# Optimization experiments

Hardware: AMD Instinct MI355X
Metric: run time of the kernel (lower is better)

The kernel has to match this reference:

```python
import jax, jax.numpy as jnp
import numpy as np


def setup_inputs() -> dict:
    key = jax.random.key(0)
    ks = jax.random.split(key, 8)
    B, T, U = 4, 400, 80
    De, Dd, V = 512, 512, 1024
    F = De + Dd  # in_features = 1024
    s = lambda k, shape: jax.random.normal(k, shape, dtype=jnp.float32) * 0.05
    return {
        "encoder_output": jax.random.normal(ks[0], (B, T, De), dtype=jnp.float32),
        "decoder_output": jax.random.normal(ks[1], (B, U, Dd), dtype=jnp.float32),
        "W_enc": s(ks[2], (F, De)),
        "b_enc": s(ks[3], (F,)),
        "W_dec": s(ks[4], (F, Dd)),
        "b_dec": s(ks[5], (F,)),
        "W_fc": s(ks[6], (V, F)),
        "b_fc": s(ks[7], (V,)),
    }


def reference(encoder_output, decoder_output, W_enc, b_enc, W_dec, b_dec, W_fc, b_fc):
    # fc_enc / fc_dec projections: (B,T,F) and (B,U,F)
    enc = jnp.einsum("btd,fd->btf", encoder_output, W_enc) + b_enc
    dec = jnp.einsum("bud,fd->buf", decoder_output, W_dec) + b_dec
    # broadcast-add -> (B,T,U,F)
    combined = enc[:, :, None, :] + dec[:, None, :, :]
    # fc: tanh then linear -> (B,T,U,V)
    vocab_logits = jnp.einsum("btuf,vf->btuv", jnp.tanh(combined), W_fc) + b_fc
    # HAT branch: blank prob via sigmoid of logit 0
    blk_logit = vocab_logits[..., :1]
    log_blk = jax.nn.log_sigmoid(blk_logit)          # log(sigmoid)
    log_not_blk = jax.nn.log_sigmoid(-blk_logit)     # log(1 - sigmoid)
    vocab_log_probs = log_not_blk + jax.nn.log_softmax(vocab_logits[..., 1:], axis=-1)
    return jnp.concatenate([log_blk, vocab_log_probs], axis=-1)
```

## Files before the change

kernel.cpp:

```cpp
#include <hip/hip_runtime.h>
#include <hip/hip_bf16.h>
#include <cstdint>
#include <cstddef>

typedef short bf16x8 __attribute__((ext_vector_type(8)));
typedef float f32x4 __attribute__((ext_vector_type(4)));

static __device__ __forceinline__ unsigned short f2bf(float f) {
    union { float f; uint32_t u; } c; c.f = f;
    uint32_t r = c.u + 0x7FFFu + ((c.u >> 16) & 1u);
    return (unsigned short)(r >> 16);
}
static __device__ __forceinline__ float bf2f_lo(uint32_t w) {
    union { uint32_t u; float f; } c; c.u = w << 16; return c.f;
}
static __device__ __forceinline__ float bf2f_hi(uint32_t w) {
    union { uint32_t u; float f; } c; c.u = w & 0xffff0000u; return c.f;
}
static __device__ __forceinline__ float fast_tanh(float x) {
    float e = __expf(2.0f * x);
    return 1.0f - 2.0f / (e + 1.0f);
}
static __device__ __forceinline__ float softplus_f(float x) {
    return fmaxf(x, 0.0f) + log1pf(__expf(-fabsf(x)));
}

#define GLOAD_LDS16(g, l) \
    __builtin_amdgcn_global_load_lds((const __attribute__((address_space(1))) void*)(g), \
                                     (__attribute__((address_space(3))) void*)(l), 16, 0, 0)

__global__ __launch_bounds__(256) void k_convert(
    const float* __restrict__ s0, const float* __restrict__ s1,
    const float* __restrict__ s2, const float* __restrict__ s3,
    const float* __restrict__ s4,
    unsigned short* __restrict__ d0, unsigned short* __restrict__ d1,
    unsigned short* __restrict__ d2, unsigned short* __restrict__ d3,
    unsigned short* __restrict__ d4,
    int n0, int n1, int n2, int n3, int n4)
{
    int i = blockIdx.x * 256 + threadIdx.x;
    int c0 = n0 >> 2, c1 = c0 + (n1 >> 2), c2 = c1 + (n2 >> 2),
        c3 = c2 + (n3 >> 2), c4 = c3 + (n4 >> 2);
    if (i >= c4) return;
    const float* s; unsigned short* d; int j;
    if (i < c0)      { s = s0; d = d0; j = i; }
    else if (i < c1) { s = s1; d = d1; j = i - c0; }
    else if (i < c2) { s = s2; d = d2; j = i - c1; }
    else if (i < c3) { s = s3; d = d3; j = i - c2; }
    else             { s = s4; d = d4; j = i - c3; }
    float4 v = reinterpret_cast<const float4*>(s)[j];
    ushort4 o;
    o.x = f2bf(v.x); o.y = f2bf(v.y); o.z = f2bf(v.z); o.w = f2bf(v.w);
    reinterpret_cast<ushort4*>(d)[j] = o;
}

__global__ __launch_bounds__(256) void k_proj(
    const unsigned short* __restrict__ A,
    const unsigned short* __restrict__ W,
    const float* __restrict__ bias,
    float* __restrict__ out)
{
    __shared__ unsigned short As[32 * 512];
    const int tid = threadIdx.x;
    const int m0 = blockIdx.x * 32;
    const int c0 = blockIdx.y * 128;
    {
        int row = tid >> 3;
        const unsigned short* src = A + (size_t)(m0 + row) * 512;
        unsigned int base = row * 1024;
        unsigned int sw = (row & 7) << 4;
        #pragma unroll
        for (int c = 0; c < 8; ++c) {
            int col = (tid & 7) * 8 + c * 64;
            bf16x8 v = *reinterpret_cast<const bf16x8*>(src + col);
            *reinterpret_cast<bf16x8*>(
                reinterpret_cast<char*>(As) + ((base + col * 2) ^ sw)) = v;
        }
    }
    __syncthreads();
    const int w = tid >> 6, l = tid & 63;
    const int lr = l & 15, lkb = (l >> 4) * 8;
    f32x4 acc[2][2] = {};
    const int colbase = c0 + w * 32;
    const unsigned short* Wb = W + (size_t)(colbase + lr) * 512 + lkb;
    const unsigned int sw = (lr & 7) << 4;
    for (int ks = 0; ks < 16; ++ks) {
        unsigned int kb = (ks * 32 + lkb) * 2;
        bf16x8 a0 = *reinterpret_cast<const bf16x8*>(
            reinterpret_cast<const char*>(As) + ((lr * 1024 + kb) ^ sw));
        bf16x8 a1 = *reinterpret_cast<const bf16x8*>(
            reinterpret_cast<const char*>(As) + (((16 + lr) * 1024 + kb) ^ sw));
        #pragma unroll
        for (int nf = 0; nf < 2; ++nf) {
            bf16x8 b = *reinterpret_cast<const bf16x8*>(Wb + nf * 16 * 512 + ks * 32);
            acc[0][nf] = __builtin_amdgcn_mfma_f32_16x16x32_bf16(a0, b, acc[0][nf], 0, 0, 0);
            acc[1][nf] = __builtin_amdgcn_mfma_f32_16x16x32_bf16(a1, b, acc[1][nf], 0, 0, 0);
        }
    }
    const int qr = (l >> 4) * 4;
    #pragma unroll
    for (int nf = 0; nf < 2; ++nf) {
        int col = colbase + nf * 16 + lr;
        float bv = bias[col];
        #pragma unroll
        for (int mf = 0; mf < 2; ++mf)
            #pragma unroll
            for (int r = 0; r < 4; ++r)
                out[(size_t)(m0 + mf * 16 + qr + r) * 1024 + col] = acc[mf][nf][r] + bv;
    }
}

__global__ __launch_bounds__(256) void k_tanhA(
    const float* __restrict__ enc_f,
    const float* __restrict__ dec_f,
    char* __restrict__ outb)
{
    const int NG = 128000 * 128;
    for (int g = blockIdx.x * 256 + threadIdx.x; g < NG; g += gridDim.x * 256) {
        int row = g >> 7, c8 = g & 127;
        int bt = row / 80;
        int u = row - bt * 80;
        int b = bt / 400;
        const float* ep = enc_f + (size_t)bt * 1024 + c8 * 8;
        const float* dp = dec_f + (size_t)(b * 80 + u) * 1024 + c8 * 8;
        float4 e0 = *(const float4*)ep, e1 = *(const float4*)(ep + 4);
        float4 f0 = *(const float4*)dp, f1 = *(const float4*)(dp + 4);
        uint4 pk;
        pk.x = (uint32_t)f2bf(fast_tanh(e0.x + f0.x)) | ((uint32_t)f2bf(fast_tanh(e0.y + f0.y)) << 16);
        pk.y = (uint32_t)f2bf(fast_tanh(e0.z + f0.z)) | ((uint32_t)f2bf(fast_tanh(e0.w + f0.w)) << 16);
        pk.z = (uint32_t)f2bf(fast_tanh(e1.x + f1.x)) | ((uint32_t)f2bf(fast_tanh(e1.y + f1.y)) << 16);
        pk.w = (uint32_t)f2bf(fast_tanh(e1.z + f1.z)) | ((uint32_t)f2bf(fast_tanh(e1.w + f1.w)) << 16);
        *(uint4*)(outb + (size_t)row * 4096 + c8 * 16) = pk;
    }
}

__global__ __launch_bounds__(512, 1) void k_gemm(
    const unsigned short* __restrict__ Wfc,
    const float* __restrict__ bfc,
    char* __restrict__ outb)
{
    extern __shared__ char smem[];
    const int tid = threadIdx.x;
    const int w = tid >> 6, l = tid & 63;
    const int lr = l & 15, q = l >> 4;
    const int wm = w >> 2, wn = w & 3;

    const int bid = (int)blockIdx.x;
    const int g = (bid & 7) * 250 + (bid >> 3);
    const size_t R0 = (size_t)(g >> 2) * 256;
    const int n0 = (g & 3) * 256;

    const unsigned kb0 = (unsigned)(((tid & 7) * 16) ^ (((tid >> 3) & 7) << 4));
    const int row0 = tid >> 3;
    const char* sA = outb + (R0 + row0) * 4096 + kb0;
    const char* sB = (const char*)Wfc + (size_t)(n0 + row0) * 2048 + kb0;
    char* const dbase = smem + tid * 16;

#define STG_A(buf, T) do { \
    const char* _a = sA + (T) * 128; char* _d = dbase + (buf); \
    GLOAD_LDS16(_a,          _d);          \
    GLOAD_LDS16(_a + 262144, _d + 8192);   \
    GLOAD_LDS16(_a + 524288, _d + 16384);  \
    GLOAD_LDS16(_a + 786432, _d + 24576);  \
} while (0)
#define STG_B01(buf, T) do { const char* _b = sB + (T) * 128; char* _d = dbase + (buf); \
    GLOAD_LDS16(_b,          _d + 32768); GLOAD_LDS16(_b + 131072, _d + 40960); } while (0)
#define STG_B23(buf, T) do { const char* _b = sB + (T) * 128; char* _d = dbase + (buf); \
    GLOAD_LDS16(_b + 262144, _d + 49152); GLOAD_LDS16(_b + 393216, _d + 57344); } while (0)

    const unsigned key = (unsigned)((lr & 7) << 4);
    const unsigned kx0 = (unsigned)(q * 16) ^ key;
    const unsigned kx1 = (unsigned)(q * 16 + 64) ^ key;
    const unsigned abase = (unsigned)((wm * 128 + lr) * 128);
    const unsigned bbase = (unsigned)(32768 + (wn * 64 + lr) * 128);

    f32x4 acc[8][4] = {};
    bf16x8 af[4][2], bf[4][2];

#define LDA(h) do { \
    _Pragma("unroll") \
    for (int mf = 0; mf < 4; ++mf) { \
        const char* _p = smem + cb + abase + (h) * 8192 + mf * 2048; \
        af[mf][0] = *(const bf16x8*)(_p + kx0); \
        af[mf][1] = *(const bf16x8*)(_p + kx1); \
    } } while (0)
#define LDB(gg) do { \
    _Pragma("unroll") \
    for (int j = 0; j < 2; ++j) { \
        const char* _p = smem + cb + bbase + ((gg) * 2 + j) * 2048; \
        bf[(gg) * 2 + j][0] = *(const bf16x8*)(_p + kx0); \
        bf[(gg) * 2 + j][1] = *(const bf16x8*)(_p + kx1); \
    } } while (0)
#define MFQ(h, gg) do { \
    __builtin_amdgcn_s_setprio(1); \
    _Pragma("unroll") \
    for (int j = 0; j < 2; ++j) \
        _Pragma("unroll") \
        for (int ks = 0; ks < 2; ++ks) \
            _Pragma("unroll") \
            for (int mf = 0; mf < 4; ++mf) \
                acc[(h) * 4 + mf][(gg) * 2 + j] = __builtin_amdgcn_mfma_f32_16x16x32_bf16( \
                    bf[(gg) * 2 + j][ks], af[mf][ks], acc[(h) * 4 + mf][(gg) * 2 + j], 0, 0, 0); \
    __builtin_amdgcn_s_setprio(0); \
} while (0)
#define BAR __builtin_amdgcn_s_barrier()

    STG_A(0u, 0);
    STG_B01(0u, 0);
    STG_B23(0u, 0);
    STG_A(65536u, 1);
    asm volatile("s_waitcnt vmcnt(4)" ::: "memory");
    BAR;
    __builtin_amdgcn_sched_barrier(0);

    #pragma unroll 2
    for (int t = 0; t < 16; ++t) {
        const unsigned cb = (unsigned)(t & 1) * 65536u;
        const unsigned nb = cb ^ 65536u;
        const bool s1 = (t + 1 < 16), s2 = (t + 2 < 16);
        LDA(0); LDB(0);
        BAR;
        MFQ(0, 0);
        LDB(1);
        if (s1) STG_B01(nb, t + 1);
        BAR;
        MFQ(0, 1);
        LDA(1);
        if (s1) STG_B23(nb, t + 1);
        BAR;
        MFQ(1, 1);
        BAR;
        if (s2) STG_A(cb, t + 2);
        MFQ(1, 0);
        if (t < 14) {
            asm volatile("s_waitcnt vmcnt(4)" ::: "memory");
            BAR;
            __builtin_amdgcn_sched_barrier(0);
        } else if (t == 14) {
            asm volatile("s_waitcnt vmcnt(0)" ::: "memory");
            BAR;
            __builtin_amdgcn_sched_barrier(0);
        }
    }
#undef LDA
#undef LDB
#undef MFQ
#undef BAR
#undef STG_A
#undef STG_B01
#undef STG_B23

    #pragma unroll
    for (int nf = 0; nf < 4; ++nf) {
        const int v = n0 + wn * 64 + nf * 16 + q * 4;
        float4 bv = *(const float4*)(bfc + v);
        #pragma unroll
        for (int mf8 = 0; mf8 < 8; ++mf8) {
            f32x4 a = acc[mf8][nf];
            uint2 pk;
            pk.x = (uint32_t)f2bf(a[0] + bv.x) | ((uint32_t)f2bf(a[1] + bv.y) << 16);
            pk.y = (uint32_t)f2bf(a[2] + bv.z) | ((uint32_t)f2bf(a[3] + bv.w) << 16);
            size_t m = R0 + (size_t)(wm * 128 + mf8 * 16 + lr);
            *(uint2*)(outb + m * 4096 + 2048 + (size_t)v * 2) = pk;
        }
    }
}

__global__ __launch_bounds__(256) void k_softmax(char* __restrict__ outb)
{
    const int row = blockIdx.x * 4 + (threadIdx.x >> 6);
    const int l = threadIdx.x & 63;
    const char* lp = outb + (size_t)row * 4096 + 2048 + l * 32;
    uint4 wa = *(const uint4*)lp;
    uint4 wb = *(const uint4*)(lp + 16);
    float v[16];
    uint32_t wd[8] = { wa.x, wa.y, wa.z, wa.w, wb.x, wb.y, wb.z, wb.w };
    #pragma unroll
    for (int i = 0; i < 8; ++i) { v[2*i] = bf2f_lo(wd[i]); v[2*i+1] = bf2f_hi(wd[i]); }

    float l0 = __shfl(v[0], 0);
    float m = (l == 0) ? -3.0e38f : v[0];
    #pragma unroll
    for (int i = 1; i < 16; ++i) m = fmaxf(m, v[i]);
    #pragma unroll
    for (int s = 1; s < 64; s <<= 1) m = fmaxf(m, __shfl_xor(m, s));
    float s = (l == 0) ? 0.0f : __expf(v[0] - m);
    #pragma unroll
    for (int i = 1; i < 16; ++i) s += __expf(v[i] - m);
    #pragma unroll
    for (int sh = 1; sh < 64; sh <<= 1) s += __shfl_xor(s, sh);

    float lse = m + __logf(s);
    float fin = -lse - softplus_f(l0);
    float f0v = -softplus_f(-l0);

    float* op = (float*)(outb + (size_t)row * 4096) + l * 16;
    #pragma unroll
    for (int c = 0; c < 4; ++c) {
        float4 o;
        o.x = v[4*c+0] + fin; o.y = v[4*c+1] + fin;
        o.z = v[4*c+2] + fin; o.w = v[4*c+3] + fin;
        if (l == 0 && c == 0) o.x = f0v;
        *(float4*)(op + 4*c) = o;
    }
}

extern "C" void kernel_launch(void* const* d_in, const int* in_sizes, int n_in,
                              void* d_out, int out_size, void* d_ws, size_t ws_size,
                              hipStream_t stream)
{
    const float* encoder = (const float*)d_in[0];
    const float* decoder = (const float*)d_in[1];
    const float* W_enc   = (const float*)d_in[2];
    const float* b_enc   = (const float*)d_in[3];
    const float* W_dec   = (const float*)d_in[4];
    const float* b_dec   = (const float*)d_in[5];
    const float* W_fc    = (const float*)d_in[6];
    const float* b_fc    = (const float*)d_in[7];
    char* outb = (char*)d_out;

    char* ws = (char*)d_ws;
    float*          enc_f  = (float*)(ws);
    float*          dec_f  = (float*)(ws + 6553600);
    unsigned short* Wfc_h  = (unsigned short*)(ws + 7864320);
    unsigned short* Wenc_h = (unsigned short*)(ws + 9961472);
    unsigned short* Wdec_h = (unsigned short*)(ws + 11010048);
    unsigned short* encI_h = (unsigned short*)(ws + 12058624);
    unsigned short* decI_h = (unsigned short*)(ws + 13697024);

    const int nEnc = 4 * 400 * 512, nDec = 4 * 80 * 512;
    const int nWe = 1024 * 512, nWd = 1024 * 512, nWf = 1024 * 1024;
    const int totalF4 = (nEnc + nDec + nWe + nWd + nWf) >> 2;
    k_convert<<<(totalF4 + 255) / 256, 256, 0, stream>>>(
        encoder, decoder, W_enc, W_dec, W_fc,
        encI_h, decI_h, Wenc_h, Wdec_h, Wfc_h,
        nEnc, nDec, nWe, nWd, nWf);

    k_proj<<<dim3(1600 / 32, 8), 256, 0, stream>>>(encI_h, Wenc_h, b_enc, enc_f);
    k_proj<<<dim3(320 / 32, 8), 256, 0, stream>>>(decI_h, Wdec_h, b_dec, dec_f);

    k_tanhA<<<4096, 256, 0, stream>>>(enc_f, dec_f, outb);

    const int GEMM_SMEM = 131072;
    hipFuncSetAttribute(reinterpret_cast<const void*>(k_gemm),
                        hipFuncAttributeMaxDynamicSharedMemorySize, GEMM_SMEM);
    k_gemm<<<2000, 512, GEMM_SMEM, stream>>>(Wfc_h, b_fc, outb);

    k_softmax<<<32000, 256, 0, stream>>>(outb);
}
```

Baseline: 660.3 us.

## Double GEMM waves per block with smaller per-wave tiles; nontemporal softmax stores

Raises the GEMM block from 512 to 1024 threads. Each of the 16 waves now computes a 64x64 sub-tile of the 256x256 block tile instead of 128x64, and global-to-LDS staging and fragment loads are redistributed to match. The aim is more waves per CU to hide LDS and MFMA latency, at the cost of more barrier participants and a tighter per-thread register budget from the launch bound, which could cause spills. The softmax output write also switches to nontemporal stores to reduce cache pollution.

Measured after the change: 887.8 us. 34.5% more time.

```diff
diff --git a/kernel.cpp b/kernel.cpp
--- a/kernel.cpp
+++ b/kernel.cpp
@@ -134,7 +134,7 @@
     }
 }
 
-__global__ __launch_bounds__(512, 1) void k_gemm(
+__global__ __launch_bounds__(1024, 2) void k_gemm(
     const unsigned short* __restrict__ Wfc,
     const float* __restrict__ bfc,
     char* __restrict__ outb)
@@ -150,66 +150,63 @@
     const size_t R0 = (size_t)(g >> 2) * 256;
     const int n0 = (g & 3) * 256;
 
-    const unsigned kb0 = (unsigned)(((tid & 7) * 16) ^ (((tid >> 3) & 7) << 4));
-    const int row0 = tid >> 3;
-    const char* sA = outb + (R0 + row0) * 4096 + kb0;
-    const char* sB = (const char*)Wfc + (size_t)(n0 + row0) * 2048 + kb0;
+    const char* sA[2]; const char* sB[2];
+    #pragma unroll
+    for (int i = 0; i < 2; ++i) {
+        unsigned d = (unsigned)tid * 16 + i * 16384;
+        unsigned L = d ^ (((d >> 7) & 7u) << 4);
+        unsigned row = L >> 7, kb = L & 127u;
+        sA[i] = outb + (R0 + row) * 4096 + kb;
+        sB[i] = (const char*)Wfc + (size_t)(n0 + row) * 2048 + kb;
+    }
     char* const dbase = smem + tid * 16;
 
 #define STG_A(buf, T) do { \
-    const char* _a = sA + (T) * 128; char* _d = dbase + (buf); \
-    GLOAD_LDS16(_a,          _d);          \
-    GLOAD_LDS16(_a + 262144, _d + 8192);   \
-    GLOAD_LDS16(_a + 524288, _d + 16384);  \
-    GLOAD_LDS16(_a + 786432, _d + 24576);  \
+    GLOAD_LDS16(sA[0] + (T) * 128, dbase + (buf)); \
+    GLOAD_LDS16(sA[1] + (T) * 128, dbase + (buf) + 16384); \
 } while (0)
-#define STG_B01(buf, T) do { const char* _b = sB + (T) * 128; char* _d = dbase + (buf); \
-    GLOAD_LDS16(_b,          _d + 32768); GLOAD_LDS16(_b + 131072, _d + 40960); } while (0)
-#define STG_B23(buf, T) do { const char* _b = sB + (T) * 128; char* _d = dbase + (buf); \
-    GLOAD_LDS16(_b + 262144, _d + 49152); GLOAD_LDS16(_b + 393216, _d + 57344); } while (0)
+#define STG_B0(buf, T) do { \
+    GLOAD_LDS16(sB[0] + (T) * 128, dbase + (buf) + 32768); } while (0)
+#define STG_B1(buf, T) do { \
+    GLOAD_LDS16(sB[1] + (T) * 128, dbase + (buf) + 49152); } while (0)
 
     const unsigned key = (unsigned)((lr & 7) << 4);
     const unsigned kx0 = (unsigned)(q * 16) ^ key;
     const unsigned kx1 = (unsigned)(q * 16 + 64) ^ key;
-    const unsigned abase = (unsigned)((wm * 128 + lr) * 128);
+    const unsigned abase = (unsigned)((wm * 64 + lr) * 128);
     const unsigned bbase = (unsigned)(32768 + (wn * 64 + lr) * 128);
 
-    f32x4 acc[8][4] = {};
-    bf16x8 af[4][2], bf[4][2];
+    f32x4 acc[4][4] = {};
+    bf16x8 af[4], bfr[2];
 
 #define LDA(h) do { \
+    const unsigned _kx = (h) ? kx1 : kx0; \
     _Pragma("unroll") \
-    for (int mf = 0; mf < 4; ++mf) { \
-        const char* _p = smem + cb + abase + (h) * 8192 + mf * 2048; \
-        af[mf][0] = *(const bf16x8*)(_p + kx0); \
-        af[mf][1] = *(const bf16x8*)(_p + kx1); \
-    } } while (0)
-#define LDB(gg) do { \
-    _Pragma("unroll") \
-    for (int j = 0; j < 2; ++j) { \
-        const char* _p = smem + cb + bbase + ((gg) * 2 + j) * 2048; \
-        bf[(gg) * 2 + j][0] = *(const bf16x8*)(_p + kx0); \
-        bf[(gg) * 2 + j][1] = *(const bf16x8*)(_p + kx1); \
-    } } while (0)
-#define MFQ(h, gg) do { \
+    for (int mf = 0; mf < 4; ++mf) \
+        af[mf] = *(const bf16x8*)(smem + cb + abase + mf * 2048 + _kx); \
+} while (0)
+#define LDB2(h, gg) do { \
+    const unsigned _kx = (h) ? kx1 : kx0; \
+    bfr[0] = *(const bf16x8*)(smem + cb + bbase + ((gg) * 2 + 0) * 2048 + _kx); \
+    bfr[1] = *(const bf16x8*)(smem + cb + bbase + ((gg) * 2 + 1) * 2048 + _kx); \
+} while (0)
+#define MFQ(gg) do { \
     __builtin_amdgcn_s_setprio(1); \
     _Pragma("unroll") \
     for (int j = 0; j < 2; ++j) \
         _Pragma("unroll") \
-        for (int ks = 0; ks < 2; ++ks) \
-            _Pragma("unroll") \
-            for (int mf = 0; mf < 4; ++mf) \
-                acc[(h) * 4 + mf][(gg) * 2 + j] = __builtin_amdgcn_mfma_f32_16x16x32_bf16( \
-                    bf[(gg) * 2 + j][ks], af[mf][ks], acc[(h) * 4 + mf][(gg) * 2 + j], 0, 0, 0); \
+        for (int mf = 0; mf < 4; ++mf) \
+            acc[mf][(gg) * 2 + j] = __builtin_amdgcn_mfma_f32_16x16x32_bf16( \
+                bfr[j], af[mf], acc[mf][(gg) * 2 + j], 0, 0, 0); \
     __builtin_amdgcn_s_setprio(0); \
 } while (0)
 #define BAR __builtin_amdgcn_s_barrier()
 
     STG_A(0u, 0);
-    STG_B01(0u, 0);
-    STG_B23(0u, 0);
+    STG_B0(0u, 0);
+    STG_B1(0u, 0);
     STG_A(65536u, 1);
-    asm volatile("s_waitcnt vmcnt(4)" ::: "memory");
+    asm volatile("s_waitcnt vmcnt(2)" ::: "memory");
     BAR;
     __builtin_amdgcn_sched_barrier(0);
 
@@ -218,22 +215,23 @@
         const unsigned cb = (unsigned)(t & 1) * 65536u;
         const unsigned nb = cb ^ 65536u;
         const bool s1 = (t + 1 < 16), s2 = (t + 2 < 16);
-        LDA(0); LDB(0);
+        LDA(0); LDB2(0, 0);
         BAR;
-        MFQ(0, 0);
-        LDB(1);
-        if (s1) STG_B01(nb, t + 1);
+        MFQ(0);
+        LDB2(0, 1);
+        if (s1) STG_B0(nb, t + 1);
         BAR;
-        MFQ(0, 1);
-        LDA(1);
-        if (s1) STG_B23(nb, t + 1);
+        MFQ(1);
+        LDA(1); LDB2(1, 1);
+        if (s1) STG_B1(nb, t + 1);
         BAR;
-        MFQ(1, 1);
+        MFQ(1);
+        LDB2(1, 0);
         BAR;
         if (s2) STG_A(cb, t + 2);
-        MFQ(1, 0);
+        MFQ(0);
         if (t < 14) {
-            asm volatile("s_waitcnt vmcnt(4)" ::: "memory");
+            asm volatile("s_waitcnt vmcnt(2)" ::: "memory");
             BAR;
             __builtin_amdgcn_sched_barrier(0);
         } else if (t == 14) {
@@ -243,24 +241,24 @@
         }
     }
 #undef LDA
-#undef LDB
+#undef LDB2
 #undef MFQ
 #undef BAR
 #undef STG_A
-#undef STG_B01
-#undef STG_B23
+#undef STG_B0
+#undef STG_B1
 
     #pragma unroll
     for (int nf = 0; nf < 4; ++nf) {
         const int v = n0 + wn * 64 + nf * 16 + q * 4;
         float4 bv = *(const float4*)(bfc + v);
         #pragma unroll
-        for (int mf8 = 0; mf8 < 8; ++mf8) {
-            f32x4 a = acc[mf8][nf];
+        for (int mf = 0; mf < 4; ++mf) {
+            f32x4 a = acc[mf][nf];
             uint2 pk;
             pk.x = (uint32_t)f2bf(a[0] + bv.x) | ((uint32_t)f2bf(a[1] + bv.y) << 16);
             pk.y = (uint32_t)f2bf(a[2] + bv.z) | ((uint32_t)f2bf(a[3] + bv.w) << 16);
-            size_t m = R0 + (size_t)(wm * 128 + mf8 * 16 + lr);
+            size_t m = R0 + (size_t)(wm * 64 + mf * 16 + lr);
             *(uint2*)(outb + m * 4096 + 2048 + (size_t)v * 2) = pk;
         }
     }
@@ -297,11 +295,11 @@
     float* op = (float*)(outb + (size_t)row * 4096) + l * 16;
     #pragma unroll
     for (int c = 0; c < 4; ++c) {
-        float4 o;
-        o.x = v[4*c+0] + fin; o.y = v[4*c+1] + fin;
-        o.z = v[4*c+2] + fin; o.w = v[4*c+3] + fin;
-        if (l == 0 && c == 0) o.x = f0v;
-        *(float4*)(op + 4*c) = o;
+        f32x4 o;
+        o[0] = v[4*c+0] + fin; o[1] = v[4*c+1] + fin;
+        o[2] = v[4*c+2] + fin; o[3] = v[4*c+3] + fin;
+        if (l == 0 && c == 0) o[0] = f0v;
+        __builtin_nontemporal_store(o, (f32x4*)(op + 4*c));
     }
 }
 
@@ -344,7 +342,7 @@
     const int GEMM_SMEM = 131072;
     hipFuncSetAttribute(reinterpret_cast<const void*>(k_gemm),
                         hipFuncAttributeMaxDynamicSharedMemorySize, GEMM_SMEM);
-    k_gemm<<<2000, 512, GEMM_SMEM, stream>>>(Wfc_h, b_fc, outb);
+    k_gemm<<<2000, 1024, GEMM_SMEM, stream>>>(Wfc_h, b_fc, outb);
 
     k_softmax<<<32000, 256, 0, stream>>>(outb);
 }
```

## Restructure GEMM main loop with register double-buffered fragments and two waves per SIMD

Applied to the files above, without the earlier changes.

Rewrites the k_gemm pipeline so that A/B fragments for the next K-step are read from LDS during the current step, using separate register sets and a ping-pong B buffer. Global-to-LDS staging is regrouped into split A halves and a full B load, issued two tiles ahead, with adjusted vmcnt waits. Launch bounds change from 1 to 2 blocks per CU to allow more occupancy. The risks are higher register pressure under the tighter bound, which could cause spills given the 128 fp32 accumulators plus fragments, and more barriers per iteration. Two blocks at 128KB LDS each may also not fit on a CU, which would make the occupancy hint moot.

Measured after the change: 1.104 ms. 1.67x slower.

```diff
diff --git a/kernel.cpp b/kernel.cpp
--- a/kernel.cpp
+++ b/kernel.cpp
@@ -134,7 +134,7 @@
     }
 }
 
-__global__ __launch_bounds__(512, 1) void k_gemm(
+__global__ __launch_bounds__(512, 2) void k_gemm(
     const unsigned short* __restrict__ Wfc,
     const float* __restrict__ bfc,
     char* __restrict__ outb)
@@ -152,21 +152,27 @@
 
     const unsigned kb0 = (unsigned)(((tid & 7) * 16) ^ (((tid >> 3) & 7) << 4));
     const int row0 = tid >> 3;
-    const char* sA = outb + (R0 + row0) * 4096 + kb0;
-    const char* sB = (const char*)Wfc + (size_t)(n0 + row0) * 2048 + kb0;
+    const char* sA0 = outb + (R0 + row0) * 4096 + kb0;
+    const char* sB0 = (const char*)Wfc + (size_t)(n0 + row0) * 2048 + kb0;
     char* const dbase = smem + tid * 16;
 
-#define STG_A(buf, T) do { \
-    const char* _a = sA + (T) * 128; char* _d = dbase + (buf); \
-    GLOAD_LDS16(_a,          _d);          \
-    GLOAD_LDS16(_a + 262144, _d + 8192);   \
-    GLOAD_LDS16(_a + 524288, _d + 16384);  \
-    GLOAD_LDS16(_a + 786432, _d + 24576);  \
+#define STG_AF(buf, T) do { \
+    const char* _g = sA0 + (size_t)(T) * 128; \
+    GLOAD_LDS16(_g,          dbase + (buf)); \
+    GLOAD_LDS16(_g + 524288, dbase + (buf) + 16384); \
 } while (0)
-#define STG_B01(buf, T) do { const char* _b = sB + (T) * 128; char* _d = dbase + (buf); \
-    GLOAD_LDS16(_b,          _d + 32768); GLOAD_LDS16(_b + 131072, _d + 40960); } while (0)
-#define STG_B23(buf, T) do { const char* _b = sB + (T) * 128; char* _d = dbase + (buf); \
-    GLOAD_LDS16(_b + 262144, _d + 49152); GLOAD_LDS16(_b + 393216, _d + 57344); } while (0)
+#define STG_AS(buf, T) do { \
+    const char* _g = sA0 + (size_t)(T) * 128; \
+    GLOAD_LDS16(_g + 262144, dbase + (buf) + 8192); \
+    GLOAD_LDS16(_g + 786432, dbase + (buf) + 24576); \
+} while (0)
+#define STG_BALL(buf, T) do { \
+    const char* _g = sB0 + (size_t)(T) * 128; \
+    GLOAD_LDS16(_g,          dbase + (buf) + 32768); \
+    GLOAD_LDS16(_g + 131072, dbase + (buf) + 40960); \
+    GLOAD_LDS16(_g + 262144, dbase + (buf) + 49152); \
+    GLOAD_LDS16(_g + 393216, dbase + (buf) + 57344); \
+} while (0)
 
     const unsigned key = (unsigned)((lr & 7) << 4);
     const unsigned kx0 = (unsigned)(q * 16) ^ key;
@@ -174,93 +180,99 @@
     const unsigned abase = (unsigned)((wm * 128 + lr) * 128);
     const unsigned bbase = (unsigned)(32768 + (wn * 64 + lr) * 128);
 
+    bf16x8 a0f[8], a1f[8];
+    bf16x8 bp0[2][4], bp1[4];
     f32x4 acc[8][4] = {};
-    bf16x8 af[4][2], bf[4][2];
-
-#define LDA(h) do { \
+
+#define RD_A(dst, h, bufb) do { \
     _Pragma("unroll") \
-    for (int mf = 0; mf < 4; ++mf) { \
-        const char* _p = smem + cb + abase + (h) * 8192 + mf * 2048; \
-        af[mf][0] = *(const bf16x8*)(_p + kx0); \
-        af[mf][1] = *(const bf16x8*)(_p + kx1); \
+    for (int mf2 = 0; mf2 < 4; ++mf2) { \
+        const char* _p = smem + (bufb) + abase + (h) * 8192 + mf2 * 2048; \
+        dst[mf2 * 2 + 0] = *(const bf16x8*)(_p + kx0); \
+        dst[mf2 * 2 + 1] = *(const bf16x8*)(_p + kx1); \
     } } while (0)
-#define LDB(gg) do { \
+#define RD_B(dst, p, bufb) do { \
     _Pragma("unroll") \
     for (int j = 0; j < 2; ++j) { \
-        const char* _p = smem + cb + bbase + ((gg) * 2 + j) * 2048; \
-        bf[(gg) * 2 + j][0] = *(const bf16x8*)(_p + kx0); \
-        bf[(gg) * 2 + j][1] = *(const bf16x8*)(_p + kx1); \
+        const char* _p = smem + (bufb) + bbase + ((p) * 2 + j) * 2048; \
+        dst[j * 2 + 0] = *(const bf16x8*)(_p + kx0); \
+        dst[j * 2 + 1] = *(const bf16x8*)(_p + kx1); \
     } } while (0)
-#define MFQ(h, gg) do { \
+#define MFQ(h, p, aset, bset) do { \
     __builtin_amdgcn_s_setprio(1); \
     _Pragma("unroll") \
     for (int j = 0; j < 2; ++j) \
         _Pragma("unroll") \
         for (int ks = 0; ks < 2; ++ks) \
             _Pragma("unroll") \
-            for (int mf = 0; mf < 4; ++mf) \
-                acc[(h) * 4 + mf][(gg) * 2 + j] = __builtin_amdgcn_mfma_f32_16x16x32_bf16( \
-                    bf[(gg) * 2 + j][ks], af[mf][ks], acc[(h) * 4 + mf][(gg) * 2 + j], 0, 0, 0); \
+            for (int mf2 = 0; mf2 < 4; ++mf2) \
+                acc[(h) * 4 + mf2][(p) * 2 + j] = __builtin_amdgcn_mfma_f32_16x16x32_bf16( \
+                    bset[j * 2 + ks], aset[mf2 * 2 + ks], acc[(h) * 4 + mf2][(p) * 2 + j], 0, 0, 0); \
     __builtin_amdgcn_s_setprio(0); \
 } while (0)
 #define BAR __builtin_amdgcn_s_barrier()
 
-    STG_A(0u, 0);
-    STG_B01(0u, 0);
-    STG_B23(0u, 0);
-    STG_A(65536u, 1);
-    asm volatile("s_waitcnt vmcnt(4)" ::: "memory");
+    STG_AF(0u, 0); STG_BALL(0u, 0); STG_AS(0u, 0);
+    STG_AF(65536u, 1); STG_BALL(65536u, 1); STG_AS(65536u, 1);
+    asm volatile("s_waitcnt vmcnt(8)" ::: "memory");
     BAR;
     __builtin_amdgcn_sched_barrier(0);
+    RD_A(a0f, 0, 0u);
+    RD_B(bp0[0], 0, 0u);
 
     #pragma unroll 2
     for (int t = 0; t < 16; ++t) {
         const unsigned cb = (unsigned)(t & 1) * 65536u;
-        const unsigned nb = cb ^ 65536u;
-        const bool s1 = (t + 1 < 16), s2 = (t + 2 < 16);
-        LDA(0); LDB(0);
-        BAR;
-        MFQ(0, 0);
-        LDB(1);
-        if (s1) STG_B01(nb, t + 1);
-        BAR;
-        MFQ(0, 1);
-        LDA(1);
-        if (s1) STG_B23(nb, t + 1);
-        BAR;
-        MFQ(1, 1);
-        BAR;
-        if (s2) STG_A(cb, t + 2);
-        MFQ(1, 0);
+        const unsigned ob = cb ^ 65536u;
+        const bool s2 = (t + 2 < 16);
+        RD_B(bp1, 1, cb);
+        BAR;
+        MFQ(0, 0, a0f, bp0[t & 1]);
+        BAR;
+        RD_A(a1f, 1, cb);
+        if (s2) STG_AF(cb, t + 2);
+        BAR;
+        MFQ(0, 1, a0f, bp1);
+        BAR;
+        if (s2) STG_BALL(cb, t + 2);
+        BAR;
+        MFQ(1, 1, a1f, bp1);
+        BAR;
         if (t < 14) {
-            asm volatile("s_waitcnt vmcnt(4)" ::: "memory");
-            BAR;
-            __builtin_amdgcn_sched_barrier(0);
-        } else if (t == 14) {
+            asm volatile("s_waitcnt vmcnt(6)" ::: "memory");
+        } else {
             asm volatile("s_waitcnt vmcnt(0)" ::: "memory");
-            BAR;
-            __builtin_amdgcn_sched_barrier(0);
-        }
-    }
-#undef LDA
-#undef LDB
+        }
+        BAR;
+        __builtin_amdgcn_sched_barrier(0);
+        if (t + 1 < 16) {
+            RD_A(a0f, 0, ob);
+            RD_B(bp0[(t + 1) & 1], 0, ob);
+        }
+        if (s2) STG_AS(cb, t + 2);
+        BAR;
+        MFQ(1, 0, a1f, bp0[t & 1]);
+        BAR;
+    }
+#undef RD_A
+#undef RD_B
 #undef MFQ
 #undef BAR
-#undef STG_A
-#undef STG_B01
-#undef STG_B23
+#undef STG_AF
+#undef STG_AS
+#undef STG_BALL
 
     #pragma unroll
     for (int nf = 0; nf < 4; ++nf) {
         const int v = n0 + wn * 64 + nf * 16 + q * 4;
         float4 bv = *(const float4*)(bfc + v);
         #pragma unroll
-        for (int mf8 = 0; mf8 < 8; ++mf8) {
-            f32x4 a = acc[mf8][nf];
+        for (int mf = 0; mf < 8; ++mf) {
+            f32x4 a = acc[mf][nf];
             uint2 pk;
             pk.x = (uint32_t)f2bf(a[0] + bv.x) | ((uint32_t)f2bf(a[1] + bv.y) << 16);
             pk.y = (uint32_t)f2bf(a[2] + bv.z) | ((uint32_t)f2bf(a[3] + bv.w) << 16);
-            size_t m = R0 + (size_t)(wm * 128 + mf8 * 16 + lr);
+            size_t m = R0 + (size_t)(wm * 128 + mf * 16 + lr);
             *(uint2*)(outb + m * 4096 + 2048 + (size_t)v * 2) = pk;
         }
     }
```
